# Performance work log

Measured on AMD Instinct MI355X. Metric: run time of the kernel, lower is better.

Reference implementation:

```python
import jax, jax.numpy as jnp
import numpy as np

B, n, A = 64, 1024, 32          # graphs, nodes/graph, actions/graph
N = B * n
EH = 2048                        # undirected edges per graph
HID, H = 128, 4
C = HID // H
NF, EF, AD, NI, L = 1, 1, 7, 4, 3
NEG_SLOPE = 0.2


def setup_inputs() -> dict:
    ks = jax.random.split(jax.random.key(0), 16)
    x = jax.random.normal(ks[0], (N, NF), jnp.float32)
    s = jax.random.randint(ks[1], (B, EH), 0, n)
    d = jax.random.randint(ks[2], (B, EH), 0, n)
    off = (jnp.arange(B) * n)[:, None]
    s = (s + off).reshape(-1)
    d = (d + off).reshape(-1)
    # bidirectional edges (unrooted trees): both i->j and j->i
    edge_index = jnp.stack([jnp.concatenate([s, d]), jnp.concatenate([d, s])]).astype(jnp.int32)
    E = edge_index.shape[1]
    edge_attr = jax.random.uniform(ks[3], (E, EF), jnp.float32)
    idx = jax.random.randint(ks[4], (B, A, NI), 0, n).astype(jnp.float32)
    meta = jax.random.normal(ks[5], (B, A, AD - NI), jnp.float32)
    action_tensor = jnp.concatenate([idx, meta], axis=-1)
    batch_idx = jnp.repeat(jnp.arange(B, dtype=jnp.int32), n)
    batch_ptr = jnp.arange(B + 1, dtype=jnp.int32) * n

    def lin(k, i, o):
        return jax.random.normal(k, (i, o), jnp.float32) / np.float32(np.sqrt(i))

    inp = dict(x=x, edge_attr=edge_attr, action_tensor=action_tensor,
               edge_index=edge_index, batch_idx=batch_idx, batch_ptr=batch_ptr)
    inp["Wn"] = lin(ks[6], NF, HID); inp["bn"] = jnp.zeros((HID,), jnp.float32)
    kl = jax.random.split(ks[7], 4 * L)
    inp["gWl"] = jnp.stack([lin(kl[i], HID, HID) for i in range(L)])
    inp["gWr"] = jnp.stack([lin(kl[L + i], HID, HID) for i in range(L)])
    inp["gWe"] = jnp.stack([lin(kl[2 * L + i], EF, HID) for i in range(L)])
    inp["gatt"] = jnp.stack([jax.random.normal(kl[3 * L + i], (H, C), jnp.float32) * 0.1 for i in range(L)])
    inp["gbl"] = jnp.zeros((L, HID), jnp.float32)
    inp["gbr"] = jnp.zeros((L, HID), jnp.float32)
    inp["gb"] = jnp.zeros((L, HID), jnp.float32)
    mlp_in = NI * HID + (AD - NI)
    inp["aW1"] = lin(ks[8], mlp_in, HID); inp["ab1"] = jnp.zeros((HID,), jnp.float32)
    inp["aW2"] = lin(ks[9], HID, HID); inp["ab2"] = jnp.zeros((HID,), jnp.float32)
    inp["qW1"] = lin(ks[10], 4 * HID, HID); inp["qb1"] = jnp.zeros((HID,), jnp.float32)
    inp["qW2"] = lin(ks[11], HID, HID); inp["qb2"] = jnp.zeros((HID,), jnp.float32)
    inp["qW3"] = lin(ks[12], HID, 1); inp["qb3"] = jnp.zeros((1,), jnp.float32)
    return inp


def _gatv2(h, src, dst, ea, Wl, bl, Wr, br, We, att, b):
    # PyG GATv2Conv: e_ij = att . leaky_relu(lin_l(x_j) + lin_r(x_i) + lin_edge(e_ij))
    Nn = h.shape[0]
    xl = (h @ Wl + bl).reshape(Nn, H, C)   # source transform
    xr = (h @ Wr + br).reshape(Nn, H, C)   # target transform
    ee = (ea @ We).reshape(-1, H, C)       # edge transform (no bias in PyG)
    e = jax.nn.leaky_relu(xl[src] + xr[dst] + ee, NEG_SLOPE)   # [E,H,C]
    logits = jnp.einsum('ehc,hc->eh', e, att)
    m = jax.ops.segment_max(logits, dst, num_segments=Nn)       # stable softmax per target node
    ex = jnp.exp(logits - m[dst])
    alpha = ex / jax.ops.segment_sum(ex, dst, num_segments=Nn)[dst]
    msg = (xl[src] * alpha[:, :, None]).reshape(-1, HID)
    return jax.ops.segment_sum(msg, dst, num_segments=Nn) + b


def reference(x, edge_attr, action_tensor, Wn, bn, gWl, gbl, gWr, gbr, gWe, gatt, gb,
              aW1, ab1, aW2, ab2, qW1, qb1, qW2, qb2, qW3, qb3,
              edge_index, batch_idx, batch_ptr):
    Nn = x.shape[0]
    nb = batch_ptr.shape[0] - 1
    # GATv2Conv default add_self_loops=True, fill_value='mean' for edge_attr
    loops = jnp.arange(Nn, dtype=edge_index.dtype)
    src = jnp.concatenate([edge_index[0], loops])
    dst = jnp.concatenate([edge_index[1], loops])
    ea = jnp.concatenate([edge_attr, jnp.broadcast_to(edge_attr.mean(0), (Nn, edge_attr.shape[1]))], 0)
    h = jax.nn.relu(x @ Wn + bn)
    for l in range(L):
        h = jax.nn.relu(_gatv2(h, src, dst, ea, gWl[l], gbl[l], gWr[l], gbr[l], gWe[l], gatt[l], gb[l])) + h
    # sum / mean / max pooling per graph
    sums = jax.ops.segment_sum(h, batch_idx, num_segments=nb)
    cnt = jax.ops.segment_sum(jnp.ones((Nn, 1), h.dtype), batch_idx, num_segments=nb)
    means = sums / cnt
    maxs = jax.ops.segment_max(h, batch_idx, num_segments=nb)
    tree_emb = jnp.concatenate([sums, means, maxs], -1)          # [B, 3*HID]
    # action encoding: gather node embeddings at action node indices (shifted by batch_ptr)
    ni = action_tensor[..., :NI].astype(jnp.int32) + batch_ptr[:-1][:, None, None]
    g = h[ni].reshape(nb, action_tensor.shape[1], NI * HID)
    ai = jnp.concatenate([g, action_tensor[..., NI:]], -1)
    ae = jax.nn.relu(jax.nn.relu(ai @ aW1 + ab1) @ aW2 + ab2)    # [B, A, HID]
    comb = jnp.concatenate([jnp.broadcast_to(tree_emb[:, None, :], (nb, ae.shape[1], 3 * HID)), ae], -1)
    q = jax.nn.relu(comb @ qW1 + qb1)
    q = jax.nn.relu(q @ qW2 + qb2)
    return (q @ qW3 + qb3).squeeze(-1)                            # [B, A]
```

## Files before the change

### kernel.cpp

```cpp
#include <hip/hip_runtime.h>
#include <hip/hip_bf16.h>

#define NNODES 65536
#define NGRAPH 64
#define NPG 1024
#define NACT 32
#define HID 128
#define NHEAD 4
#define CPH 32

typedef __attribute__((ext_vector_type(8))) short bf16x8;
typedef __attribute__((ext_vector_type(4))) float f32x4;

__device__ __forceinline__ void load32(float* dst, const float* src) {
    const float4* s4 = (const float4*)src;
#pragma unroll
    for (int i = 0; i < 8; ++i) {
        float4 q = s4[i];
        dst[i*4+0] = q.x; dst[i*4+1] = q.y; dst[i*4+2] = q.z; dst[i*4+3] = q.w;
    }
}

__device__ __forceinline__ void load8(float* dst, const float* src) {
    float4 q0 = ((const float4*)src)[0];
    float4 q1 = ((const float4*)src)[1];
    dst[0]=q0.x; dst[1]=q0.y; dst[2]=q0.z; dst[3]=q0.w;
    dst[4]=q1.x; dst[5]=q1.y; dst[6]=q1.z; dst[7]=q1.w;
}

__device__ __forceinline__ unsigned short f2bf(float f) {
    unsigned int u = __float_as_uint(f);
    u = (u + 0x7fffu + ((u >> 16) & 1u)) >> 16;
    return (unsigned short)u;
}


__global__ void reduce_mean_k(const float* __restrict__ ea, int E0, float* __restrict__ out) {
    __shared__ float s[256];
    int t = threadIdx.x;
    float acc = 0.f;
    for (int i = blockIdx.x * 256 + t; i < E0; i += gridDim.x * 256) acc += ea[i];
    s[t] = acc; __syncthreads();
    for (int off = 128; off > 0; off >>= 1) { if (t < off) s[t] += s[t+off]; __syncthreads(); }
    if (t == 0) atomicAdd(out, s[0]);
}

__global__ void hist_k(const int* __restrict__ ei, int* __restrict__ deg, int E0) {
    int e = blockIdx.x * 256 + threadIdx.x;
    if (e < E0) atomicAdd(&deg[ei[E0 + e]], 1);
}

__global__ void scan_bsum_k(const int* __restrict__ deg, int* __restrict__ bsum) {
    __shared__ int s[256];
    int t = threadIdx.x;
    s[t] = deg[blockIdx.x * 256 + t]; __syncthreads();
    for (int off = 128; off > 0; off >>= 1) { if (t < off) s[t] += s[t+off]; __syncthreads(); }
    if (t == 0) bsum[blockIdx.x] = s[0];
}

__global__ void scan_boff_k(const int* __restrict__ bsum, int* __restrict__ boff) {
    __shared__ int s[256];
    int t = threadIdx.x;
    s[t] = bsum[t]; __syncthreads();
    for (int off = 1; off < 256; off <<= 1) {
        int v = (t >= off) ? s[t-off] : 0; __syncthreads();
        s[t] += v; __syncthreads();
    }
    boff[t] = s[t] - bsum[t];
}

__global__ void scan_rowptr_k(const int* __restrict__ deg, const int* __restrict__ boff,
                              int* __restrict__ rowptr, int N, int E0) {
    __shared__ int s[256];
    int t = threadIdx.x;
    int i = blockIdx.x * 256 + t;
    int d = deg[i];
    s[t] = d; __syncthreads();
    for (int off = 1; off < 256; off <<= 1) {
        int v = (t >= off) ? s[t-off] : 0; __syncthreads();
        s[t] += v; __syncthreads();
    }
    rowptr[i] = boff[blockIdx.x] + s[t] - d;
    if (i == N - 1) rowptr[N] = E0;
}

__global__ void scatter_k(const int* __restrict__ ei, const float* __restrict__ ea,
                          const int* __restrict__ rowptr, int* __restrict__ cursor,
                          int* __restrict__ csr_src, float* __restrict__ csr_ea, int E0) {
    int e = blockIdx.x * 256 + threadIdx.x;
    if (e >= E0) return;
    int s = ei[e], d = ei[E0 + e];
    int pos = atomicAdd(&cursor[d], 1);
    int slot = rowptr[d] + pos;
    csr_src[slot] = s;
    csr_ea[slot]  = ea[e];
}

__global__ void wt_prep_k(const float* __restrict__ gWl, const float* __restrict__ gWr,
                          unsigned short* __restrict__ wtl, unsigned short* __restrict__ wtr) {
    int idx = blockIdx.x * 256 + threadIdx.x;
    int l = idx >> 14, rem = idx & 16383;
    int n = rem >> 7, k = rem & 127;
    int src = l*16384 + k*128 + n;
    wtl[idx] = f2bf(gWl[src]);
    wtr[idx] = f2bf(gWr[src]);
}

__global__ void mlp_prep_k(const float* __restrict__ aW1, const float* __restrict__ aW2,
                           const float* __restrict__ qW1, const float* __restrict__ qW2,
                           unsigned short* __restrict__ wA1t, unsigned short* __restrict__ wA2t,
                           unsigned short* __restrict__ wQ1t, unsigned short* __restrict__ wQ2t) {
    int n = blockIdx.x;
    int t = threadIdx.x;
    for (int k = t; k < 544; k += 256)
        wA1t[n*544 + k] = (k < 515) ? f2bf(aW1[(size_t)k*128 + n]) : (unsigned short)0;
    if (t < 128) {
        wA2t[n*128 + t] = f2bf(aW2[(size_t)t*128 + n]);
        wQ1t[n*128 + t] = f2bf(qW1[(size_t)(384 + t)*128 + n]);
        wQ2t[n*128 + t] = f2bf(qW2[(size_t)t*128 + n]);
    }
}

__global__ void node_init_k(const float* __restrict__ x, const float* __restrict__ Wn,
                            const float* __restrict__ bn, float* __restrict__ h,
                            unsigned short* __restrict__ hb) {
    int idx = blockIdx.x * 256 + threadIdx.x;
    int i = idx >> 7, f = idx & 127;
    float v = x[i] * Wn[f] + bn[f];
    v = v > 0.f ? v : 0.f;
    h[idx] = v;
    hb[idx] = f2bf(v);
}

__global__ __launch_bounds__(256) void gemm_lr_mfma_k(
    const unsigned short* __restrict__ hb,
    const unsigned short* __restrict__ wtl, const unsigned short* __restrict__ wtr,
    const float* __restrict__ bl, const float* __restrict__ br,
    float* __restrict__ xl, float* __restrict__ xr) {
    int wave = threadIdx.x >> 6;
    int lane = threadIdx.x & 63;
    int lr = lane & 15;
    int lq = lane >> 4;
    int r0 = blockIdx.x * 128 + wave * 32;

    const short* hs = (const short*)hb;
    bf16x8 a[2][4];
#pragma unroll
    for (int rt = 0; rt < 2; ++rt)
#pragma unroll
        for (int kf = 0; kf < 4; ++kf)
            a[rt][kf] = *(const bf16x8*)(hs + (size_t)(r0 + rt*16 + lr)*HID + kf*32 + lq*8);

    const short* ws[2]   = {(const short*)wtl, (const short*)wtr};
    const float* bias[2] = {bl, br};
    float* outp[2]       = {xl, xr};

#pragma unroll
    for (int m = 0; m < 2; ++m) {
        const short* W = ws[m];
        f32x4 acc[2][8];
#pragma unroll
        for (int rt = 0; rt < 2; ++rt)
#pragma unroll
            for (int ct = 0; ct < 8; ++ct) acc[rt][ct] = (f32x4){0.f,0.f,0.f,0.f};

        bf16x8 b[4], nb[4];
#pragma unroll
        for (int kf = 0; kf < 4; ++kf)
            b[kf] = *(const bf16x8*)(W + (size_t)(lr)*HID + kf*32 + lq*8);
#pragma unroll
        for (int ct = 0; ct < 8; ++ct) {
            if (ct < 7) {
#pragma unroll
                for (int kf = 0; kf < 4; ++kf)
                    nb[kf] = *(const bf16x8*)(W + (size_t)((ct+1)*16 + lr)*HID + kf*32 + lq*8);
            }
#pragma unroll
            for (int rt = 0; rt < 2; ++rt)
#pragma unroll
                for (int kf = 0; kf < 4; ++kf)
                    acc[rt][ct] = __builtin_amdgcn_mfma_f32_16x16x32_bf16(a[rt][kf], b[kf], acc[rt][ct], 0, 0, 0);
#pragma unroll
            for (int kf = 0; kf < 4; ++kf) b[kf] = nb[kf];
        }
#pragma unroll
        for (int ct = 0; ct < 8; ++ct) {
            float bv = bias[m][ct*16 + lr];
#pragma unroll
            for (int rt = 0; rt < 2; ++rt)
#pragma unroll
                for (int rg = 0; rg < 4; ++rg) {
                    int row = r0 + rt*16 + lq*4 + rg;
                    outp[m][(size_t)row*HID + ct*16 + lr] = acc[rt][ct][rg] + bv;
                }
        }
    }
}

__global__ __launch_bounds__(256, 8) void gat_edge_k(
    const float* __restrict__ xl, const float* __restrict__ xr,
    float* __restrict__ h, unsigned short* __restrict__ hb,
    const int* __restrict__ rowptr, const int* __restrict__ csr_src,
    const float* __restrict__ csr_ea,
    const float* __restrict__ We, const float* __restrict__ att,
    const float* __restrict__ gb, const float* __restrict__ meansum, float inv_e0) {
    int xcd  = blockIdx.x & 7;
    int slot = blockIdx.x >> 3;
    int g    = xcd * 8 + (slot >> 6);
    int j    = slot & 63;
    int t    = threadIdx.x;
    int v    = g * NPG + j * 16 + (t >> 4);
    int li   = t & 15;
    int base = li * 8;
    float mea = meansum[0] * inv_e0;

    float xrv[8], attv[8], wev[8];
    load8(xrv, xr + (size_t)v*HID + base);
    load8(attv, att + base);
    load8(wev, We + base);

    float m = -1e30f, den = 0.f;
    float acc[8];
#pragma unroll
    for (int c = 0; c < 8; ++c) acc[c] = 0.f;

    int s0 = rowptr[v], s1 = rowptr[v+1];
    float an = mea;
    float xn[8];
    load8(xn, xl + (size_t)v*HID + base);
    for (int i = s0 - 1; i < s1; ++i) {
        int i2 = (i + 1 < s1) ? (i + 1) : s0;
        int s2 = csr_src[i2] & (NNODES - 1);
        float a2 = csr_ea[i2];
        float x2[8];
        load8(x2, xl + (size_t)s2*HID + base);

        float lg = 0.f;
#pragma unroll
        for (int c = 0; c < 8; ++c) {
            float e = xn[c] + xrv[c] + an * wev[c];
            e = fmaxf(e, 0.2f * e);
            lg = fmaf(attv[c], e, lg);
        }
        lg += __shfl_xor(lg, 1, 64);
        lg += __shfl_xor(lg, 2, 64);

        float mn  = fmaxf(m, lg);
        float sc  = __expf(m - mn);
        float wgt = __expf(lg - mn);
        den = den * sc + wgt;
#pragma unroll
        for (int c = 0; c < 8; ++c) acc[c] = acc[c] * sc + wgt * xn[c];
        m = mn;
        an = a2;
#pragma unroll
        for (int c = 0; c < 8; ++c) xn[c] = x2[c];
    }

    float inv = 1.f / den;
    size_t o = (size_t)v*HID + base;
    float hold[8], gbv[8];
    load8(hold, h + o);
    load8(gbv, gb + base);
    float nh[8];
#pragma unroll
    for (int c = 0; c < 8; ++c) {
        float val = acc[c] * inv + gbv[c];
        val = val > 0.f ? val : 0.f;
        nh[c] = val + hold[c];
    }
    float4* hp = (float4*)(h + o);
    hp[0] = make_float4(nh[0], nh[1], nh[2], nh[3]);
    hp[1] = make_float4(nh[4], nh[5], nh[6], nh[7]);
    unsigned int* hbp = (unsigned int*)(hb + o);
#pragma unroll
    for (int q = 0; q < 4; ++q)
        hbp[q] = (unsigned int)f2bf(nh[2*q]) | ((unsigned int)f2bf(nh[2*q+1]) << 16);
}

__global__ __launch_bounds__(256) void pool_k(const float* __restrict__ h,
                                              float* __restrict__ tree_sum,
                                              float* __restrict__ tree_max) {
    int b = blockIdx.x >> 3, chunk = blockIdx.x & 7;
    int t = threadIdx.x, col = t & 127, half = t >> 7;
    const float* hb_ = h + ((size_t)b * NPG + chunk * 128 + half * 64) * HID;
    float s = 0.f, mx = 0.f;
    for (int i = 0; i < 64; ++i) {
        float v = hb_[(size_t)i*HID + col];
        s += v; mx = fmaxf(mx, v);
    }
    __shared__ float sb[2][128], mb[2][128];
    sb[half][col] = s; mb[half][col] = mx;
    __syncthreads();
    if (half == 0) {
        s  = sb[0][col] + sb[1][col];
        mx = fmaxf(mb[0][col], mb[1][col]);
        atomicAdd(&tree_sum[b*128 + col], s);
        atomicMax((int*)&tree_max[b*128 + col], __float_as_int(mx));
    }
}

#define SA1 552
#define SAC 136
__global__ __launch_bounds__(256) void action_q_k(
    const unsigned short* __restrict__ hb, const float* __restrict__ action,
    const int* __restrict__ batch_ptr,
    const float* __restrict__ tree_sum, const float* __restrict__ tree_max,
    const unsigned short* __restrict__ wA1t, const float* __restrict__ ab1,
    const unsigned short* __restrict__ wA2t, const float* __restrict__ ab2,
    const float* __restrict__ qW1, const unsigned short* __restrict__ wQ1t,
    const float* __restrict__ qb1,
    const unsigned short* __restrict__ wQ2t, const float* __restrict__ qb2,
    const float* __restrict__ qW3, const float* __restrict__ qb3,
    float* __restrict__ out) {
    int b = blockIdx.x;
    int t = threadIdx.x;
    int w  = t >> 6;
    int lane = t & 63;
    int lr = lane & 15;
    int lq = lane >> 4;

    __shared__ unsigned short aib[32 * SA1];
    __shared__ unsigned short z1s[32 * SAC];
    __shared__ unsigned short aes[32 * SAC];
    __shared__ unsigned short q1s[32 * SAC];
    __shared__ float q2f[32 * 132];
    __shared__ float tqA[128], tqB[128];
    __shared__ float psum[32][8];

    int ptr = batch_ptr[b];

    {
        int p = t >> 1, half = t & 1;
        int a = p >> 2, j = p & 3;
        const float* actp = action + (size_t)(b * NACT + a) * 7;
        int ni = (int)actp[j] + ptr;
        const uint4* src = (const uint4*)(hb + (size_t)ni * HID) + half * 8;
        uint4* dst = (uint4*)((char*)aib + ((size_t)a * SA1 + j * 128 + half * 64) * 2);
#pragma unroll
        for (int q = 0; q < 8; ++q) dst[q] = src[q];
        if (t < 32) {
            const float* ap = action + (size_t)(b * NACT + t) * 7;
            aib[t * SA1 + 512] = f2bf(ap[4]);
            aib[t * SA1 + 513] = f2bf(ap[5]);
            aib[t * SA1 + 514] = f2bf(ap[6]);
            for (int i = 3; i < 40; ++i) aib[t * SA1 + 512 + i] = 0;
        }
    }

    {
        if (t < 128) {
            int col = t;
            float acc = 0.f;
#pragma unroll 4
            for (int k = 0; k < 128; ++k) {
                float sv = tree_sum[b * 128 + k];
                acc = fmaf(sv, qW1[(size_t)k * 128 + col], acc);
                acc = fmaf(sv * (1.f / 1024.f), qW1[(size_t)(128 + k) * 128 + col], acc);
            }
            tqA[col] = acc;
        } else {
            int col = t - 128;
            float acc = 0.f;
#pragma unroll 4
            for (int k = 0; k < 128; ++k) {
                float mv = tree_max[b * 128 + k];
                acc = fmaf(mv, qW1[(size_t)(256 + k) * 128 + col], acc);
            }
            tqB[col] = acc;
        }
    }
    __syncthreads();

    f32x4 acc[2][2];
    const unsigned short* srcA;
    int strideA, K;

    srcA = aib; strideA = SA1; K = 544;
#pragma unroll
    for (int rt = 0; rt < 2; ++rt)
#pragma unroll
        for (int ci = 0; ci < 2; ++ci) acc[rt][ci] = (f32x4){0.f, 0.f, 0.f, 0.f};
    for (int ks = 0; ks < K; ks += 32) {
        bf16x8 a0 = *(const bf16x8*)(srcA + (0 * 16 + lr) * strideA + ks + lq * 8);
        bf16x8 a1 = *(const bf16x8*)(srcA + (1 * 16 + lr) * strideA + ks + lq * 8);
        bf16x8 b0 = *(const bf16x8*)(wA1t + (size_t)((2 * w + 0) * 16 + lr) * K + ks + lq * 8);
        bf16x8 b1 = *(const bf16x8*)(wA1t + (size_t)((2 * w + 1) * 16 + lr) * K + ks + lq * 8);
        acc[0][0] = __builtin_amdgcn_mfma_f32_16x16x32_bf16(a0, b0, acc[0][0], 0, 0, 0);
        acc[0][1] = __builtin_amdgcn_mfma_f32_16x16x32_bf16(a0, b1, acc[0][1], 0, 0, 0);
        acc[1][0] = __builtin_amdgcn_mfma_f32_16x16x32_bf16(a1, b0, acc[1][0], 0, 0, 0);
        acc[1][1] = __builtin_amdgcn_mfma_f32_16x16x32_bf16(a1, b1, acc[1][1], 0, 0, 0);
    }
#pragma unroll
    for (int ci = 0; ci < 2; ++ci) {
        int col = (2 * w + ci) * 16 + lr;
        float bv = ab1[col];
#pragma unroll
        for (int rt = 0; rt < 2; ++rt)
#pragma unroll
            for (int rg = 0; rg < 4; ++rg) {
                int row = rt * 16 + lq * 4 + rg;
                z1s[row * SAC + col] = f2bf(fmaxf(acc[rt][ci][rg] + bv, 0.f));
            }
    }
    __syncthreads();

    srcA = z1s; strideA = SAC; K = 128;
#pragma unroll
    for (int rt = 0; rt < 2; ++rt)
#pragma unroll
        for (int ci = 0; ci < 2; ++ci) acc[rt][ci] = (f32x4){0.f, 0.f, 0.f, 0.f};
#pragma unroll
    for (int ks = 0; ks < 128; ks += 32) {
        bf16x8 a0 = *(const bf16x8*)(srcA + (0 * 16 + lr) * strideA + ks + lq * 8);
        bf16x8 a1 = *(const bf16x8*)(srcA + (1 * 16 + lr) * strideA + ks + lq * 8);
        bf16x8 b0 = *(const bf16x8*)(wA2t + (size_t)((2 * w + 0) * 16 + lr) * K + ks + lq * 8);
        bf16x8 b1 = *(const bf16x8*)(wA2t + (size_t)((2 * w + 1) * 16 + lr) * K + ks + lq * 8);
        acc[0][0] = __builtin_amdgcn_mfma_f32_16x16x32_bf16(a0, b0, acc[0][0], 0, 0, 0);
        acc[0][1] = __builtin_amdgcn_mfma_f32_16x16x32_bf16(a0, b1, acc[0][1], 0, 0, 0);
        acc[1][0] = __builtin_amdgcn_mfma_f32_16x16x32_bf16(a1, b0, acc[1][0], 0, 0, 0);
        acc[1][1] = __builtin_amdgcn_mfma_f32_16x16x32_bf16(a1, b1, acc[1][1], 0, 0, 0);
    }
#pragma unroll
    for (int ci = 0; ci < 2; ++ci) {
        int col = (2 * w + ci) * 16 + lr;
        float bv = ab2[col];
#pragma unroll
        for (int rt = 0; rt < 2; ++rt)
#pragma unroll
            for (int rg = 0; rg < 4; ++rg) {
                int row = rt * 16 + lq * 4 + rg;
                aes[row * SAC + col] = f2bf(fmaxf(acc[rt][ci][rg] + bv, 0.f));
            }
    }
    __syncthreads();

    srcA = aes; strideA = SAC; K = 128;
#pragma unroll
    for (int rt = 0; rt < 2; ++rt)
#pragma unroll
        for (int ci = 0; ci < 2; ++ci) acc[rt][ci] = (f32x4){0.f, 0.f, 0.f, 0.f};
#pragma unroll
    for (int ks = 0; ks < 128; ks += 32) {
        bf16x8 a0 = *(const bf16x8*)(srcA + (0 * 16 + lr) * strideA + ks + lq * 8);
        bf16x8 a1 = *(const bf16x8*)(srcA + (1 * 16 + lr) * strideA + ks + lq * 8);
        bf16x8 b0 = *(const bf16x8*)(wQ1t + (size_t)((2 * w + 0) * 16 + lr) * K + ks + lq * 8);
        bf16x8 b1 = *(const bf16x8*)(wQ1t + (size_t)((2 * w + 1) * 16 + lr) * K + ks + lq * 8);
        acc[0][0] = __builtin_amdgcn_mfma_f32_16x16x32_bf16(a0, b0, acc[0][0], 0, 0, 0);
        acc[0][1] = __builtin_amdgcn_mfma_f32_16x16x32_bf16(a0, b1, acc[0][1], 0, 0, 0);
        acc[1][0] = __builtin_amdgcn_mfma_f32_16x16x32_bf16(a1, b0, acc[1][0], 0, 0, 0);
        acc[1][1] = __builtin_amdgcn_mfma_f32_16x16x32_bf16(a1, b1, acc[1][1], 0, 0, 0);
    }
#pragma unroll
    for (int ci = 0; ci < 2; ++ci) {
        int col = (2 * w + ci) * 16 + lr;
        float bv = qb1[col] + tqA[col] + tqB[col];
#pragma unroll
        for (int rt = 0; rt < 2; ++rt)
#pragma unroll
            for (int rg = 0; rg < 4; ++rg) {
                int row = rt * 16 + lq * 4 + rg;
                q1s[row * SAC + col] = f2bf(fmaxf(acc[rt][ci][rg] + bv, 0.f));
            }
    }
    __syncthreads();

    srcA = q1s; strideA = SAC; K = 128;
#pragma unroll
    for (int rt = 0; rt < 2; ++rt)
#pragma unroll
        for (int ci = 0; ci < 2; ++ci) acc[rt][ci] = (f32x4){0.f, 0.f, 0.f, 0.f};
#pragma unroll
    for (int ks = 0; ks < 128; ks += 32) {
        bf16x8 a0 = *(const bf16x8*)(srcA + (0 * 16 + lr) * strideA + ks + lq * 8);
        bf16x8 a1 = *(const bf16x8*)(srcA + (1 * 16 + lr) * strideA + ks + lq * 8);
        bf16x8 b0 = *(const bf16x8*)(wQ2t + (size_t)((2 * w + 0) * 16 + lr) * K + ks + lq * 8);
        bf16x8 b1 = *(const bf16x8*)(wQ2t + (size_t)((2 * w + 1) * 16 + lr) * K + ks + lq * 8);
        acc[0][0] = __builtin_amdgcn_mfma_f32_16x16x32_bf16(a0, b0, acc[0][0], 0, 0, 0);
        acc[0][1] = __builtin_amdgcn_mfma_f32_16x16x32_bf16(a0, b1, acc[0][1], 0, 0, 0);
        acc[1][0] = __builtin_amdgcn_mfma_f32_16x16x32_bf16(a1, b0, acc[1][0], 0, 0, 0);
        acc[1][1] = __builtin_amdgcn_mfma_f32_16x16x32_bf16(a1, b1, acc[1][1], 0, 0, 0);
    }
#pragma unroll
    for (int ci = 0; ci < 2; ++ci) {
        int col = (2 * w + ci) * 16 + lr;
        float bv = qb2[col];
#pragma unroll
        for (int rt = 0; rt < 2; ++rt)
#pragma unroll
            for (int rg = 0; rg < 4; ++rg) {
                int row = rt * 16 + lq * 4 + rg;
                q2f[row * 132 + col] = fmaxf(acc[rt][ci][rg] + bv, 0.f);
            }
    }
    __syncthreads();

    {
        int a = t >> 3, seg = t & 7;
        float s = 0.f;
#pragma unroll
        for (int k = 0; k < 16; ++k)
            s = fmaf(q2f[a * 132 + seg * 16 + k], qW3[seg * 16 + k], s);
        psum[a][seg] = s;
    }
    __syncthreads();
    if (t < 32) {
        float s = qb3[0];
#pragma unroll
        for (int i = 0; i < 8; ++i) s += psum[t][i];
        out[(size_t)b * NACT + t] = s;
    }
}

extern "C" void kernel_launch(void* const* d_in, const int* in_sizes, int n_in,
                              void* d_out, int out_size, void* d_ws, size_t ws_size,
                              hipStream_t stream) {
    const float* x         = (const float*)d_in[0];
    const float* edge_attr = (const float*)d_in[1];
    const float* action    = (const float*)d_in[2];
    const int*   edge_idx  = (const int*)d_in[3];
    const int*   batch_ptr = (const int*)d_in[5];
    const float* Wn  = (const float*)d_in[6];
    const float* bn  = (const float*)d_in[7];
    const float* gWl = (const float*)d_in[8];
    const float* gWr = (const float*)d_in[9];
    const float* gWe = (const float*)d_in[10];
    const float* gatt= (const float*)d_in[11];
    const float* gbl = (const float*)d_in[12];
    const float* gbr = (const float*)d_in[13];
    const float* gb  = (const float*)d_in[14];
    const float* aW1 = (const float*)d_in[15];
    const float* ab1 = (const float*)d_in[16];
    const float* aW2 = (const float*)d_in[17];
    const float* ab2 = (const float*)d_in[18];
    const float* qW1 = (const float*)d_in[19];
    const float* qb1 = (const float*)d_in[20];
    const float* qW2 = (const float*)d_in[21];
    const float* qb2 = (const float*)d_in[22];
    const float* qW3 = (const float*)d_in[23];
    const float* qb3 = (const float*)d_in[24];
    float* out = (float*)d_out;

    const int E0 = in_sizes[1];
    const int N  = NNODES;

    char* w = (char*)d_ws;
    auto alloc = [&](size_t bytes) { void* p = (void*)w; w += (bytes + 255) & ~(size_t)255; return p; };
    float* h        = (float*)alloc((size_t)N * HID * 4);
    unsigned short* hb = (unsigned short*)alloc((size_t)N * HID * 2);
    float* xl       = (float*)alloc((size_t)N * HID * 4);
    float* xr       = (float*)alloc((size_t)N * HID * 4);
    int*   rowptr   = (int*)alloc((size_t)(N + 1) * 4);
    int*   deg      = (int*)alloc((size_t)N * 4);
    int*   cursor   = (int*)alloc((size_t)N * 4);
    int*   bsum     = (int*)alloc(256 * 4);
    int*   boff     = (int*)alloc(256 * 4);
    int*   csr_src  = (int*)alloc((size_t)E0 * 4);
    float* csr_ea   = (float*)alloc((size_t)E0 * 4);
    unsigned short* wtl = (unsigned short*)alloc((size_t)3*128*128*2);
    unsigned short* wtr = (unsigned short*)alloc((size_t)3*128*128*2);
    unsigned short* wA1t = (unsigned short*)alloc((size_t)128*544*2);
    unsigned short* wA2t = (unsigned short*)alloc((size_t)128*128*2);
    unsigned short* wQ1t = (unsigned short*)alloc((size_t)128*128*2);
    unsigned short* wQ2t = (unsigned short*)alloc((size_t)128*128*2);
    float* tree_sum = (float*)alloc((size_t)NGRAPH * 128 * 4);
    float* tree_max = (float*)alloc((size_t)NGRAPH * 128 * 4);
    float* meansum  = (float*)alloc(256);

    hipMemsetAsync(deg, 0, (size_t)N * 4, stream);
    hipMemsetAsync(cursor, 0, (size_t)N * 4, stream);
    hipMemsetAsync(meansum, 0, 4, stream);
    hipMemsetAsync(tree_sum, 0, (size_t)NGRAPH * 128 * 4, stream);
    hipMemsetAsync(tree_max, 0, (size_t)NGRAPH * 128 * 4, stream);

    int eb = (E0 + 255) / 256;
    reduce_mean_k<<<256, 256, 0, stream>>>(edge_attr, E0, meansum);
    hist_k<<<eb, 256, 0, stream>>>(edge_idx, deg, E0);
    scan_bsum_k<<<N/256, 256, 0, stream>>>(deg, bsum);
    scan_boff_k<<<1, 256, 0, stream>>>(bsum, boff);
    scan_rowptr_k<<<N/256, 256, 0, stream>>>(deg, boff, rowptr, N, E0);
    scatter_k<<<eb, 256, 0, stream>>>(edge_idx, edge_attr, rowptr, cursor, csr_src, csr_ea, E0);

    wt_prep_k<<<(3*128*128)/256, 256, 0, stream>>>(gWl, gWr, wtl, wtr);
    mlp_prep_k<<<128, 256, 0, stream>>>(aW1, aW2, qW1, qW2, wA1t, wA2t, wQ1t, wQ2t);
    node_init_k<<<(N * HID) / 256, 256, 0, stream>>>(x, Wn, bn, h, hb);

    float inv_e0 = 1.0f / (float)E0;
    for (int l = 0; l < 3; ++l) {
        gemm_lr_mfma_k<<<N / 128, 256, 0, stream>>>(
            hb, wtl + (size_t)l*128*128, wtr + (size_t)l*128*128,
            gbl + l*HID, gbr + l*HID, xl, xr);
        gat_edge_k<<<N / 16, 256, 0, stream>>>(
            xl, xr, h, hb, rowptr, csr_src, csr_ea,
            gWe + l*HID, gatt + l*NHEAD*CPH, gb + l*HID, meansum, inv_e0);
    }

    pool_k<<<NGRAPH * 8, 256, 0, stream>>>(h, tree_sum, tree_max);

    action_q_k<<<NGRAPH, 256, 0, stream>>>(
        hb, action, batch_ptr, tree_sum, tree_max,
        wA1t, ab1, wA2t, ab2, qW1, wQ1t, qb1, wQ2t, qb2, qW3, qb3, out);
}
```

Baseline: 378.7 us.

## Store xl in bf16, stage CSR edges in LDS, merge setup kernels

The left projection xl is now written as bf16 and unpacked in the GAT edge kernel, halving the bytes per gathered neighbour row. Each block first stages its 16 nodes' CSR source indices and edge attributes into shared memory. The self-loop term is peeled out of the edge loop. Separately, the histogram and mean-reduce kernels, the two weight-prep kernels, and the five memsets are each merged to cut launch count. The change lowers precision of xl in the attention logits and aggregated messages, and the LDS staging silently truncates if 16 nodes have more than 2048 edges.

Measured after the change: 347.1 us. 1.09x faster.

```diff
diff --git a/kernel.cpp b/kernel.cpp
--- a/kernel.cpp
+++ b/kernel.cpp
@@ -12,15 +12,6 @@
 typedef __attribute__((ext_vector_type(8))) short bf16x8;
 typedef __attribute__((ext_vector_type(4))) float f32x4;
 
-__device__ __forceinline__ void load32(float* dst, const float* src) {
-    const float4* s4 = (const float4*)src;
-#pragma unroll
-    for (int i = 0; i < 8; ++i) {
-        float4 q = s4[i];
-        dst[i*4+0] = q.x; dst[i*4+1] = q.y; dst[i*4+2] = q.z; dst[i*4+3] = q.w;
-    }
-}
-
 __device__ __forceinline__ void load8(float* dst, const float* src) {
     float4 q0 = ((const float4*)src)[0];
     float4 q1 = ((const float4*)src)[1];
@@ -28,6 +19,15 @@
     dst[4]=q1.x; dst[5]=q1.y; dst[6]=q1.z; dst[7]=q1.w;
 }
 
+__device__ __forceinline__ void load8bf(float* dst, const unsigned short* src) {
+    uint4 q = *(const uint4*)src;
+    unsigned int u0 = q.x, u1 = q.y, u2 = q.z, u3 = q.w;
+    dst[0] = __uint_as_float(u0 << 16); dst[1] = __uint_as_float(u0 & 0xffff0000u);
+    dst[2] = __uint_as_float(u1 << 16); dst[3] = __uint_as_float(u1 & 0xffff0000u);
+    dst[4] = __uint_as_float(u2 << 16); dst[5] = __uint_as_float(u2 & 0xffff0000u);
+    dst[6] = __uint_as_float(u3 << 16); dst[7] = __uint_as_float(u3 & 0xffff0000u);
+}
+
 __device__ __forceinline__ unsigned short f2bf(float f) {
     unsigned int u = __float_as_uint(f);
     u = (u + 0x7fffu + ((u >> 16) & 1u)) >> 16;
@@ -35,19 +35,19 @@
 }
 
 
-__global__ void reduce_mean_k(const float* __restrict__ ea, int E0, float* __restrict__ out) {
+__global__ void hist_mean_k(const int* __restrict__ ei, const float* __restrict__ ea,
+                            int* __restrict__ deg, float* __restrict__ meansum, int E0) {
     __shared__ float s[256];
     int t = threadIdx.x;
-    float acc = 0.f;
-    for (int i = blockIdx.x * 256 + t; i < E0; i += gridDim.x * 256) acc += ea[i];
-    s[t] = acc; __syncthreads();
+    int e = blockIdx.x * 256 + t;
+    float v = 0.f;
+    if (e < E0) {
+        atomicAdd(&deg[ei[E0 + e]], 1);
+        v = ea[e];
+    }
+    s[t] = v; __syncthreads();
     for (int off = 128; off > 0; off >>= 1) { if (t < off) s[t] += s[t+off]; __syncthreads(); }
-    if (t == 0) atomicAdd(out, s[0]);
-}
-
-__global__ void hist_k(const int* __restrict__ ei, int* __restrict__ deg, int E0) {
-    int e = blockIdx.x * 256 + threadIdx.x;
-    if (e < E0) atomicAdd(&deg[ei[E0 + e]], 1);
+    if (t == 0) atomicAdd(meansum, s[0]);
 }
 
 __global__ void scan_bsum_k(const int* __restrict__ deg, int* __restrict__ bsum) {
@@ -96,28 +96,29 @@
     csr_ea[slot]  = ea[e];
 }
 
-__global__ void wt_prep_k(const float* __restrict__ gWl, const float* __restrict__ gWr,
-                          unsigned short* __restrict__ wtl, unsigned short* __restrict__ wtr) {
-    int idx = blockIdx.x * 256 + threadIdx.x;
-    int l = idx >> 14, rem = idx & 16383;
-    int n = rem >> 7, k = rem & 127;
-    int src = l*16384 + k*128 + n;
-    wtl[idx] = f2bf(gWl[src]);
-    wtr[idx] = f2bf(gWr[src]);
-}
-
-__global__ void mlp_prep_k(const float* __restrict__ aW1, const float* __restrict__ aW2,
-                           const float* __restrict__ qW1, const float* __restrict__ qW2,
-                           unsigned short* __restrict__ wA1t, unsigned short* __restrict__ wA2t,
-                           unsigned short* __restrict__ wQ1t, unsigned short* __restrict__ wQ2t) {
-    int n = blockIdx.x;
-    int t = threadIdx.x;
-    for (int k = t; k < 544; k += 256)
-        wA1t[n*544 + k] = (k < 515) ? f2bf(aW1[(size_t)k*128 + n]) : (unsigned short)0;
-    if (t < 128) {
-        wA2t[n*128 + t] = f2bf(aW2[(size_t)t*128 + n]);
-        wQ1t[n*128 + t] = f2bf(qW1[(size_t)(384 + t)*128 + n]);
-        wQ2t[n*128 + t] = f2bf(qW2[(size_t)t*128 + n]);
+__global__ void prep_k(const float* __restrict__ gWl, const float* __restrict__ gWr,
+                       unsigned short* __restrict__ wtl, unsigned short* __restrict__ wtr,
+                       const float* __restrict__ aW1, const float* __restrict__ aW2,
+                       const float* __restrict__ qW1, const float* __restrict__ qW2,
+                       unsigned short* __restrict__ wA1t, unsigned short* __restrict__ wA2t,
+                       unsigned short* __restrict__ wQ1t, unsigned short* __restrict__ wQ2t) {
+    int bid = blockIdx.x, t = threadIdx.x;
+    if (bid < 192) {
+        int idx = bid * 256 + t;
+        int l = idx >> 14, rem = idx & 16383;
+        int n = rem >> 7, k = rem & 127;
+        int src = l*16384 + k*128 + n;
+        wtl[idx] = f2bf(gWl[src]);
+        wtr[idx] = f2bf(gWr[src]);
+    } else {
+        int n = bid - 192;
+        for (int k = t; k < 544; k += 256)
+            wA1t[n*544 + k] = (k < 515) ? f2bf(aW1[(size_t)k*128 + n]) : (unsigned short)0;
+        if (t < 128) {
+            wA2t[n*128 + t] = f2bf(aW2[(size_t)t*128 + n]);
+            wQ1t[n*128 + t] = f2bf(qW1[(size_t)(384 + t)*128 + n]);
+            wQ2t[n*128 + t] = f2bf(qW2[(size_t)t*128 + n]);
+        }
     }
 }
 
@@ -136,7 +137,7 @@
     const unsigned short* __restrict__ hb,
     const unsigned short* __restrict__ wtl, const unsigned short* __restrict__ wtr,
     const float* __restrict__ bl, const float* __restrict__ br,
-    float* __restrict__ xl, float* __restrict__ xr) {
+    unsigned short* __restrict__ xlb, float* __restrict__ xr) {
     int wave = threadIdx.x >> 6;
     int lane = threadIdx.x & 63;
     int lr = lane & 15;
@@ -153,7 +154,6 @@
 
     const short* ws[2]   = {(const short*)wtl, (const short*)wtr};
     const float* bias[2] = {bl, br};
-    float* outp[2]       = {xl, xr};
 
 #pragma unroll
     for (int m = 0; m < 2; ++m) {
@@ -191,70 +191,98 @@
 #pragma unroll
                 for (int rg = 0; rg < 4; ++rg) {
                     int row = r0 + rt*16 + lq*4 + rg;
-                    outp[m][(size_t)row*HID + ct*16 + lr] = acc[rt][ct][rg] + bv;
+                    float val = acc[rt][ct][rg] + bv;
+                    if (m == 0) xlb[(size_t)row*HID + ct*16 + lr] = f2bf(val);
+                    else        xr [(size_t)row*HID + ct*16 + lr] = val;
                 }
         }
     }
 }
 
 __global__ __launch_bounds__(256, 8) void gat_edge_k(
-    const float* __restrict__ xl, const float* __restrict__ xr,
+    const unsigned short* __restrict__ xlb, const float* __restrict__ xr,
     float* __restrict__ h, unsigned short* __restrict__ hb,
     const int* __restrict__ rowptr, const int* __restrict__ csr_src,
     const float* __restrict__ csr_ea,
     const float* __restrict__ We, const float* __restrict__ att,
     const float* __restrict__ gb, const float* __restrict__ meansum, float inv_e0) {
+    __shared__ int   s_src[2048];
+    __shared__ float s_ea[2048];
     int xcd  = blockIdx.x & 7;
     int slot = blockIdx.x >> 3;
     int g    = xcd * 8 + (slot >> 6);
     int j    = slot & 63;
     int t    = threadIdx.x;
-    int v    = g * NPG + j * 16 + (t >> 4);
+    int vb   = g * NPG + j * 16;
+    int v    = vb + (t >> 4);
     int li   = t & 15;
     int base = li * 8;
     float mea = meansum[0] * inv_e0;
+
+    int span0 = rowptr[vb];
+    int cnt   = rowptr[vb + 16] - span0;
+    for (int i = t; i < cnt && i < 2048; i += 256) {
+        s_src[i] = csr_src[span0 + i];
+        s_ea[i]  = csr_ea[span0 + i];
+    }
+    __syncthreads();
 
     float xrv[8], attv[8], wev[8];
     load8(xrv, xr + (size_t)v*HID + base);
     load8(attv, att + base);
     load8(wev, We + base);
 
-    float m = -1e30f, den = 0.f;
-    float acc[8];
-#pragma unroll
-    for (int c = 0; c < 8; ++c) acc[c] = 0.f;
-
-    int s0 = rowptr[v], s1 = rowptr[v+1];
-    float an = mea;
-    float xn[8];
-    load8(xn, xl + (size_t)v*HID + base);
-    for (int i = s0 - 1; i < s1; ++i) {
-        int i2 = (i + 1 < s1) ? (i + 1) : s0;
-        int s2 = csr_src[i2] & (NNODES - 1);
-        float a2 = csr_ea[i2];
-        float x2[8];
-        load8(x2, xl + (size_t)s2*HID + base);
-
+    float acc[8], xn[8];
+    load8bf(xn, xlb + (size_t)v*HID + base);
+    float m;
+    {
         float lg = 0.f;
 #pragma unroll
         for (int c = 0; c < 8; ++c) {
-            float e = xn[c] + xrv[c] + an * wev[c];
+            float e = xn[c] + xrv[c] + mea * wev[c];
             e = fmaxf(e, 0.2f * e);
             lg = fmaf(attv[c], e, lg);
         }
         lg += __shfl_xor(lg, 1, 64);
         lg += __shfl_xor(lg, 2, 64);
-
-        float mn  = fmaxf(m, lg);
-        float sc  = __expf(m - mn);
-        float wgt = __expf(lg - mn);
-        den = den * sc + wgt;
-#pragma unroll
-        for (int c = 0; c < 8; ++c) acc[c] = acc[c] * sc + wgt * xn[c];
-        m = mn;
-        an = a2;
-#pragma unroll
-        for (int c = 0; c < 8; ++c) xn[c] = x2[c];
+        m = lg;
+#pragma unroll
+        for (int c = 0; c < 8; ++c) acc[c] = xn[c];
+    }
+    float den = 1.f;
+
+    int s0 = rowptr[v] - span0, s1 = rowptr[v+1] - span0;
+    if (s0 < s1) {
+        float an = s_ea[s0];
+        load8bf(xn, xlb + (size_t)s_src[s0]*HID + base);
+        for (int i = s0; i < s1; ++i) {
+            int i2 = (i + 1 < s1) ? (i + 1) : s0;
+            int   sidx2 = s_src[i2];
+            float a2    = s_ea[i2];
+            float x2[8];
+            load8bf(x2, xlb + (size_t)sidx2*HID + base);
+
+            float lg = 0.f;
+#pragma unroll
+            for (int c = 0; c < 8; ++c) {
+                float e = xn[c] + xrv[c] + an * wev[c];
+                e = fmaxf(e, 0.2f * e);
+                lg = fmaf(attv[c], e, lg);
+            }
+            lg += __shfl_xor(lg, 1, 64);
+            lg += __shfl_xor(lg, 2, 64);
+
+            float mn  = fmaxf(m, lg);
+            float sc  = __expf(m - mn);
+            float wgt = __expf(lg - mn);
+            den = den * sc + wgt;
+#pragma unroll
+            for (int c = 0; c < 8; ++c) acc[c] = acc[c] * sc + wgt * xn[c];
+            m = mn;
+            an = a2;
+#pragma unroll
+            for (int c = 0; c < 8; ++c) xn[c] = x2[c];
+        }
     }
 
     float inv = 1.f / den;
@@ -547,12 +575,16 @@
     char* w = (char*)d_ws;
     auto alloc = [&](size_t bytes) { void* p = (void*)w; w += (bytes + 255) & ~(size_t)255; return p; };
     float* h        = (float*)alloc((size_t)N * HID * 4);
-    unsigned short* hb = (unsigned short*)alloc((size_t)N * HID * 2);
-    float* xl       = (float*)alloc((size_t)N * HID * 4);
+    unsigned short* hb  = (unsigned short*)alloc((size_t)N * HID * 2);
+    unsigned short* xlb = (unsigned short*)alloc((size_t)N * HID * 2);
     float* xr       = (float*)alloc((size_t)N * HID * 4);
     int*   rowptr   = (int*)alloc((size_t)(N + 1) * 4);
     int*   deg      = (int*)alloc((size_t)N * 4);
     int*   cursor   = (int*)alloc((size_t)N * 4);
+    float* meansum  = (float*)alloc(256);
+    float* tree_sum = (float*)alloc((size_t)NGRAPH * 128 * 4);
+    float* tree_max = (float*)alloc((size_t)NGRAPH * 128 * 4);
+    size_t zero_span = (size_t)((char*)(tree_max + NGRAPH * 128) - (char*)deg);
     int*   bsum     = (int*)alloc(256 * 4);
     int*   boff     = (int*)alloc(256 * 4);
     int*   csr_src  = (int*)alloc((size_t)E0 * 4);
@@ -563,35 +595,27 @@
     unsigned short* wA2t = (unsigned short*)alloc((size_t)128*128*2);
     unsigned short* wQ1t = (unsigned short*)alloc((size_t)128*128*2);
     unsigned short* wQ2t = (unsigned short*)alloc((size_t)128*128*2);
-    float* tree_sum = (float*)alloc((size_t)NGRAPH * 128 * 4);
-    float* tree_max = (float*)alloc((size_t)NGRAPH * 128 * 4);
-    float* meansum  = (float*)alloc(256);
-
-    hipMemsetAsync(deg, 0, (size_t)N * 4, stream);
-    hipMemsetAsync(cursor, 0, (size_t)N * 4, stream);
-    hipMemsetAsync(meansum, 0, 4, stream);
-    hipMemsetAsync(tree_sum, 0, (size_t)NGRAPH * 128 * 4, stream);
-    hipMemsetAsync(tree_max, 0, (size_t)NGRAPH * 128 * 4, stream);
+
+    hipMemsetAsync(deg, 0, zero_span, stream);
 
     int eb = (E0 + 255) / 256;
-    reduce_mean_k<<<256, 256, 0, stream>>>(edge_attr, E0, meansum);
-    hist_k<<<eb, 256, 0, stream>>>(edge_idx, deg, E0);
+    hist_mean_k<<<eb, 256, 0, stream>>>(edge_idx, edge_attr, deg, meansum, E0);
     scan_bsum_k<<<N/256, 256, 0, stream>>>(deg, bsum);
     scan_boff_k<<<1, 256, 0, stream>>>(bsum, boff);
     scan_rowptr_k<<<N/256, 256, 0, stream>>>(deg, boff, rowptr, N, E0);
     scatter_k<<<eb, 256, 0, stream>>>(edge_idx, edge_attr, rowptr, cursor, csr_src, csr_ea, E0);
 
-    wt_prep_k<<<(3*128*128)/256, 256, 0, stream>>>(gWl, gWr, wtl, wtr);
-    mlp_prep_k<<<128, 256, 0, stream>>>(aW1, aW2, qW1, qW2, wA1t, wA2t, wQ1t, wQ2t);
+    prep_k<<<320, 256, 0, stream>>>(gWl, gWr, wtl, wtr,
+                                    aW1, aW2, qW1, qW2, wA1t, wA2t, wQ1t, wQ2t);
     node_init_k<<<(N * HID) / 256, 256, 0, stream>>>(x, Wn, bn, h, hb);
 
     float inv_e0 = 1.0f / (float)E0;
     for (int l = 0; l < 3; ++l) {
         gemm_lr_mfma_k<<<N / 128, 256, 0, stream>>>(
             hb, wtl + (size_t)l*128*128, wtr + (size_t)l*128*128,
-            gbl + l*HID, gbr + l*HID, xl, xr);
+            gbl + l*HID, gbr + l*HID, xlb, xr);
         gat_edge_k<<<N / 16, 256, 0, stream>>>(
-            xl, xr, h, hb, rowptr, csr_src, csr_ea,
+            xlb, xr, h, hb, rowptr, csr_src, csr_ea,
             gWe + l*HID, gatt + l*NHEAD*CPH, gb + l*HID, meansum, inv_e0);
     }
 
```
